# Optimization experiments

Measured on AMD Instinct MI355X. Metric: run time of the kernel, lower is better.

Reference implementation:

```python
import jax, jax.numpy as jnp
import numpy as np


def setup_inputs() -> dict:
    key = jax.random.key(0)
    ks = jax.random.split(key, 6)
    bs, n_src, n_tgt = 4, 4096, 16384
    c_src, c_tgt = 256, 128
    xyz_target = jax.random.uniform(ks[0], (bs, n_tgt, 3), dtype=jnp.float32)
    xyz_source = jax.random.uniform(ks[1], (bs, n_src, 3), dtype=jnp.float32)
    feats_target = jax.random.normal(ks[2], (bs, n_tgt, c_tgt), dtype=jnp.float32)
    feats_source = jax.random.normal(ks[3], (bs, n_src, c_src), dtype=jnp.float32)
    # SharedMlP 1x1 conv weights (1,1,cin,cout) squeezed to (cin,cout)
    w1 = jax.random.normal(ks[4], (c_src + c_tgt, 256), dtype=jnp.float32) * (1.0 / np.sqrt(c_src + c_tgt))
    w2 = jax.random.normal(ks[5], (256, 256), dtype=jnp.float32) * (1.0 / np.sqrt(256))
    return {"xyz_target": xyz_target, "xyz_source": xyz_source,
            "feats_target": feats_target, "feats_source": feats_source,
            "w1": w1, "w2": w2}


def reference(xyz_target, xyz_source, feats_target, feats_source, w1, w2):
    # --- three_nn: full pairwise euclidean distance [bs, n_tgt, n_src] ---
    diff = xyz_target[:, :, None, :] - xyz_source[:, None, :, :]
    dis = jnp.linalg.norm(diff, axis=-1)                      # bs, n_tgt, n_src
    neg_dis, idx = jax.lax.top_k(-dis, 3)                     # 3 nearest
    nn_dis = jnp.maximum(-neg_dis, 1e-10)                     # bs, n_tgt, 3
    inv = 1.0 / nn_dis
    weight = inv / jnp.sum(inv, axis=-1, keepdims=True)       # bs, n_tgt, 3
    # --- three_interpolate: batched gather + weighted reduce ---
    feats_sel = jax.vmap(lambda f, i: f[i])(feats_source, idx)  # bs, n_tgt, 3, c
    w_sum = jnp.sum(weight, axis=-1, keepdims=True) + 1e-6
    interp = jnp.einsum('btk,btkc->btc', weight, feats_sel) / w_sum
    # --- concat skip features, 1x1-conv MLP (pointwise matmul) ---
    x = jnp.concatenate([interp, feats_target], axis=2)       # bs, n_tgt, 384
    x = jax.nn.relu(jnp.einsum('btc,cd->btd', x, w1))
    x = jax.nn.relu(jnp.einsum('btc,cd->btd', x, w2))
    return x
```

## Files before the change

### kernel.cpp

```cpp
#include <hip/hip_runtime.h>
#include <hip/hip_bf16.h>
#include <stdint.h>

#define BS 4
#define NS 4096
#define NT 16384
#define CS 256
#define CT 128
#define KC1 384
#define NOUT 256
#define MTOT (BS*NT)
#define GR 8
#define NC (GR*GR*GR)
#define HCELL 0.125f

typedef __attribute__((ext_vector_type(4))) float floatx4;
typedef __attribute__((ext_vector_type(8))) short shortx8;
typedef __attribute__((ext_vector_type(8))) __bf16 bf16x8;

__device__ __forceinline__ unsigned short f2bf(float f) {
  unsigned int u = __builtin_bit_cast(unsigned int, f);
  u += 0x7FFFu + ((u >> 16) & 1u);
  return (unsigned short)(u >> 16);
}

__device__ __forceinline__ int cell_of(float x) {
  int c = (int)(x * 8.0f);
  return min(7, max(0, c));
}

__global__ __launch_bounds__(256) void wt_kernel(const float* __restrict__ w1,
    const float* __restrict__ w2, unsigned short* __restrict__ w1t,
    unsigned short* __restrict__ w2t) {
  int i = blockIdx.x * 256 + threadIdx.x;
  if (i < KC1 * NOUT) {
    int n = i / KC1, k = i - n * KC1;
    w1t[i] = f2bf(w1[k * NOUT + n]);
  }
  if (i < NOUT * NOUT) {
    int n = i >> 8, k = i & 255;
    w2t[i] = f2bf(w2[k * NOUT + n]);
  }
}

__global__ __launch_bounds__(512) void bucket_src(const float* __restrict__ xyzs,
    float4* __restrict__ bsrc, int* __restrict__ soff) {
  __shared__ int cnt[NC];
  __shared__ int scan[NC];
  int tid = threadIdx.x;
  int b = blockIdx.x;
  const float* src = xyzs + (size_t)b * NS * 3;
  cnt[tid] = 0;
  __syncthreads();
  #pragma unroll
  for (int k = 0; k < 8; ++k) {
    int p = k * 512 + tid;
    float x = src[3*p], y = src[3*p+1], z = src[3*p+2];
    int c = (cell_of(z) * GR + cell_of(y)) * GR + cell_of(x);
    atomicAdd(&cnt[c], 1);
  }
  __syncthreads();
  scan[tid] = cnt[tid];
  __syncthreads();
  for (int off = 1; off < NC; off <<= 1) {
    int v = (tid >= off) ? scan[tid - off] : 0;
    __syncthreads();
    scan[tid] += v;
    __syncthreads();
  }
  int excl = scan[tid] - cnt[tid];
  cnt[tid] = excl;
  soff[b * (NC + 1) + tid] = excl;
  if (tid == 0) soff[b * (NC + 1) + NC] = NS;
  __syncthreads();
  #pragma unroll
  for (int k = 0; k < 8; ++k) {
    int p = k * 512 + tid;
    float x = src[3*p], y = src[3*p+1], z = src[3*p+2];
    int c = (cell_of(z) * GR + cell_of(y)) * GR + cell_of(x);
    int slot = atomicAdd(&cnt[c], 1);
    bsrc[(size_t)b * NS + slot] = make_float4(x, y, z, __int_as_float(p));
  }
}

__global__ __launch_bounds__(1024) void sort_tgt(const float* __restrict__ xyzt,
    float4* __restrict__ stgt) {
  __shared__ int cnt[NC];
  __shared__ int scan[NC];
  int tid = threadIdx.x;
  int b = blockIdx.x;
  const float* tp = xyzt + (size_t)b * NT * 3;
  if (tid < NC) cnt[tid] = 0;
  __syncthreads();
  #pragma unroll
  for (int k = 0; k < 16; ++k) {
    int p = k * 1024 + tid;
    float x = tp[3*p], y = tp[3*p+1], z = tp[3*p+2];
    int c = (cell_of(z) * GR + cell_of(y)) * GR + cell_of(x);
    atomicAdd(&cnt[c], 1);
  }
  __syncthreads();
  if (tid < NC) scan[tid] = cnt[tid];
  __syncthreads();
  for (int off = 1; off < NC; off <<= 1) {
    int v = (tid < NC && tid >= off) ? scan[tid - off] : 0;
    __syncthreads();
    if (tid < NC) scan[tid] += v;
    __syncthreads();
  }
  if (tid < NC) cnt[tid] = scan[tid] - cnt[tid];
  __syncthreads();
  #pragma unroll
  for (int k = 0; k < 16; ++k) {
    int p = k * 1024 + tid;
    float x = tp[3*p], y = tp[3*p+1], z = tp[3*p+2];
    int c = (cell_of(z) * GR + cell_of(y)) * GR + cell_of(x);
    int slot = atomicAdd(&cnt[c], 1);
    stgt[(size_t)b * NT + slot] = make_float4(x, y, z, __int_as_float(p));
  }
}

__device__ __forceinline__ void ins3(float sc, int jj,
    float& d0, float& d1, float& d2, int& i0, int& i1, int& i2) {
  bool l0 = sc < d0, l1 = sc < d1, l2 = sc < d2;
  d2 = l1 ? d1 : (l2 ? sc : d2);
  i2 = l1 ? i1 : (l2 ? jj : i2);
  d1 = l0 ? d0 : (l1 ? sc : d1);
  i1 = l0 ? i0 : (l1 ? jj : i1);
  d0 = l0 ? sc : d0;
  i0 = l0 ? jj : i0;
}

__device__ __forceinline__ void pair_merge(float& d0, float& d1, float& d2,
                                           int& i0, int& i1, int& i2,
                                           int delta, int sub) {
  float e0 = __shfl_xor(d0, delta);
  float e1 = __shfl_xor(d1, delta);
  float e2 = __shfl_xor(d2, delta);
  int   y0 = __shfl_xor(i0, delta);
  int   y1 = __shfl_xor(i1, delta);
  int   y2 = __shfl_xor(i2, delta);
  float a0,a1,a2,b0,b1,b2; int x0,x1,x2,z0,z1,z2;
  if ((sub & delta) == 0) { a0=d0;a1=d1;a2=d2; x0=i0;x1=i1;x2=i2;
                            b0=e0;b1=e1;b2=e2; z0=y0;z1=y1;z2=y2; }
  else                    { a0=e0;a1=e1;a2=e2; x0=y0;x1=y1;x2=y2;
                            b0=d0;b1=d1;b2=d2; z0=i0;z1=i1;z2=i2; }
  bool t = a0 <= b0;
  d0 = t ? a0 : b0; i0 = t ? x0 : z0;
  float na0 = t ? a1 : a0; int nx0 = t ? x1 : x0;
  float na1 = t ? a2 : a1; int nx1 = t ? x2 : x1;
  float nb0 = t ? b0 : b1; int nz0 = t ? z0 : z1;
  float nb1 = t ? b1 : b2; int nz1 = t ? z1 : z2;
  t = na0 <= nb0;
  d1 = t ? na0 : nb0; i1 = t ? nx0 : nz0;
  float ma0 = t ? na1 : na0; int mx0 = t ? nx1 : nx0;
  float mb0 = t ? nb0 : nb1; int mz0 = t ? nz0 : nz1;
  t = ma0 <= mb0;
  d2 = t ? ma0 : mb0; i2 = t ? mx0 : mz0;
}

__global__ __launch_bounds__(256) void nn_kernel(const float4* __restrict__ stgt,
    const float4* __restrict__ bsrc, const int* __restrict__ soff,
    int* __restrict__ idx_out, float* __restrict__ w_out) {
  __shared__ float4 s_src[NS];
  __shared__ int s_off[NC + 1];
  int tid = threadIdx.x;
  int b = blockIdx.x >> 7;
  int tseg = blockIdx.x & 127;
  for (int i = tid; i < NS; i += 256) s_src[i] = bsrc[(size_t)b * NS + i];
  for (int i = tid; i < NC + 1; i += 256) s_off[i] = soff[b * (NC + 1) + i];
  __syncthreads();
  int tpair = tid >> 1, half = tid & 1;
  float4 tg = stgt[(size_t)b * NT + tseg * 128 + tpair];
  float tx = tg.x, ty = tg.y, tz = tg.z;
  int orig = __float_as_int(tg.w);
  int cx = cell_of(tx), cy = cell_of(ty), cz = cell_of(tz);
  int wx = min(max(cx, 1), 6) - 1;
  int wy = min(max(cy, 1), 6) - 1;
  int wz = min(max(cz, 1), 6) - 1;
  float d0 = 1e30f, d1 = 1e30f, d2 = 1e30f;
  int i0 = 0, i1 = 0, i2 = 0;
  for (int r = half; r < 9; r += 2) {
    int ez = wz + r / 3, ey = wy + r % 3;
    int rowc = (ez * GR + ey) * GR + wx;
    int lo = s_off[rowc], hi = s_off[rowc + 3];
    for (int p = lo; p < hi; ++p) {
      float4 s = s_src[p];
      float dx = tx - s.x, dy = ty - s.y, dz = tz - s.z;
      float q = dx*dx + dy*dy + dz*dz;
      ins3(q, __float_as_int(s.w), d0, d1, d2, i0, i1, i2);
    }
  }
  pair_merge(d0, d1, d2, i0, i1, i2, 1, half);
  float clx = fminf(wx > 0 ? tx - wx * HCELL : 1e30f,
                    wx + 3 < GR ? (wx + 3) * HCELL - tx : 1e30f);
  float cly = fminf(wy > 0 ? ty - wy * HCELL : 1e30f,
                    wy + 3 < GR ? (wy + 3) * HCELL - ty : 1e30f);
  float clz = fminf(wz > 0 ? tz - wz * HCELL : 1e30f,
                    wz + 3 < GR ? (wz + 3) * HCELL - tz : 1e30f);
  float cl = fminf(clx, fminf(cly, clz));
  bool bad = d2 > cl * cl;
  if (__any(bad)) {
    if (bad) {
      d0 = d1 = d2 = 1e30f; i0 = i1 = i2 = 0;
      for (int p = half; p < NS; p += 2) {
        float4 s = s_src[p];
        float dx = tx - s.x, dy = ty - s.y, dz = tz - s.z;
        float q = dx*dx + dy*dy + dz*dz;
        ins3(q, __float_as_int(s.w), d0, d1, d2, i0, i1, i2);
      }
    }
    pair_merge(d0, d1, d2, i0, i1, i2, 1, half);
  }
  if (half == 0) {
    float r0 = fmaxf(sqrtf(d0), 1e-10f);
    float r1 = fmaxf(sqrtf(d1), 1e-10f);
    float r2 = fmaxf(sqrtf(d2), 1e-10f);
    float v0 = 1.f/r0, v1 = 1.f/r1, v2 = 1.f/r2;
    float sc = 1.f / ((v0 + v1 + v2) * (1.f + 1e-6f));
    size_t o = ((size_t)b * NT + orig) * 3;
    idx_out[o] = i0; idx_out[o+1] = i1; idx_out[o+2] = i2;
    w_out[o] = v0*sc; w_out[o+1] = v1*sc; w_out[o+2] = v2*sc;
  }
}

__global__ __launch_bounds__(256) void build_x(const float* __restrict__ ft,
    const float* __restrict__ fs, const int* __restrict__ idxb,
    const float* __restrict__ wgtb, unsigned short* __restrict__ X) {
  int row = blockIdx.x * 4 + (threadIdx.x >> 6);
  int lane = threadIdx.x & 63;
  int b = row >> 14;
  int t = row & (NT - 1);
  const int* ip = idxb + (size_t)row * 3;
  const float* wp = wgtb + (size_t)row * 3;
  int i0 = ip[0], i1 = ip[1], i2 = ip[2];
  float w0 = wp[0], w1 = wp[1], w2 = wp[2];
  const float* fsb = fs + (size_t)b * NS * CS;
  float4 a = *((const float4*)(fsb + (size_t)i0 * CS) + lane);
  float4 c = *((const float4*)(fsb + (size_t)i1 * CS) + lane);
  float4 e = *((const float4*)(fsb + (size_t)i2 * CS) + lane);
  float4 v;
  v.x = w0*a.x + w1*c.x + w2*e.x;
  v.y = w0*a.y + w1*c.y + w2*e.y;
  v.z = w0*a.z + w1*c.z + w2*e.z;
  v.w = w0*a.w + w1*c.w + w2*e.w;
  unsigned short* xr = X + (size_t)row * KC1;
  ushort4 pk; pk.x = f2bf(v.x); pk.y = f2bf(v.y); pk.z = f2bf(v.z); pk.w = f2bf(v.w);
  *(ushort4*)(xr + lane*4) = pk;
  float2 tv = *((const float2*)(ft + ((size_t)b*NT + t)*CT) + lane);
  ushort2 pk2; pk2.x = f2bf(tv.x); pk2.y = f2bf(tv.y);
  *(ushort2*)(xr + CS + lane*2) = pk2;
}

template<int K, bool OUT_BF16>
__global__ __launch_bounds__(256) void mlp_gemm(const unsigned short* __restrict__ A,
    const unsigned short* __restrict__ Bt, void* __restrict__ Cout) {
  constexpr int LDT = 72;
  __shared__ __attribute__((aligned(16))) short sA[128 * LDT];
  __shared__ __attribute__((aligned(16))) short sB[128 * LDT];
  int tid = threadIdx.x;
  int m0 = blockIdx.x * 128;
  int n0 = blockIdx.y * 128;
  int wave = tid >> 6, lane = tid & 63;
  int wm = (wave >> 1) * 64, wn = (wave & 1) * 64;
  int fr = lane & 15, quad = lane >> 4;
  floatx4 zero = {0.f, 0.f, 0.f, 0.f};
  floatx4 acc[4][4];
  #pragma unroll
  for (int i = 0; i < 4; ++i)
    #pragma unroll
    for (int j = 0; j < 4; ++j) acc[i][j] = zero;

  for (int kt = 0; kt < K; kt += 64) {
    #pragma unroll
    for (int i = 0; i < 4; ++i) {
      int chunk = tid + 256 * i;
      int r = chunk >> 3, kc = chunk & 7;
      *(shortx8*)&sA[r * LDT + kc * 8] =
          *(const shortx8*)(A + (size_t)(m0 + r) * K + kt + kc * 8);
      *(shortx8*)&sB[r * LDT + kc * 8] =
          *(const shortx8*)(Bt + (size_t)(n0 + r) * K + kt + kc * 8);
    }
    __syncthreads();
    #pragma unroll
    for (int kk = 0; kk < 64; kk += 32) {
      bf16x8 af[4], bfr[4];
      #pragma unroll
      for (int mi = 0; mi < 4; ++mi)
        af[mi] = __builtin_bit_cast(bf16x8,
            *(const shortx8*)&sA[(wm + mi*16 + fr)*LDT + kk + quad*8]);
      #pragma unroll
      for (int ni = 0; ni < 4; ++ni)
        bfr[ni] = __builtin_bit_cast(bf16x8,
            *(const shortx8*)&sB[(wn + ni*16 + fr)*LDT + kk + quad*8]);
      #pragma unroll
      for (int mi = 0; mi < 4; ++mi)
        #pragma unroll
        for (int ni = 0; ni < 4; ++ni)
          acc[mi][ni] = __builtin_amdgcn_mfma_f32_16x16x32_bf16(
              af[mi], bfr[ni], acc[mi][ni], 0, 0, 0);
    }
    __syncthreads();
  }
  #pragma unroll
  for (int mi = 0; mi < 4; ++mi) {
    #pragma unroll
    for (int ni = 0; ni < 4; ++ni) {
      #pragma unroll
      for (int r = 0; r < 4; ++r) {
        int grow = m0 + wm + mi*16 + quad*4 + r;
        int gcol = n0 + wn + ni*16 + fr;
        float v = fmaxf(acc[mi][ni][r], 0.f);
        if constexpr (OUT_BF16)
          ((unsigned short*)Cout)[(size_t)grow * NOUT + gcol] = f2bf(v);
        else
          ((float*)Cout)[(size_t)grow * NOUT + gcol] = v;
      }
    }
  }
}

extern "C" void kernel_launch(void* const* d_in, const int* in_sizes, int n_in,
                              void* d_out, int out_size, void* d_ws, size_t ws_size,
                              hipStream_t stream) {
  (void)in_sizes; (void)n_in; (void)out_size; (void)ws_size;
  const float* xyzt = (const float*)d_in[0];
  const float* xyzs = (const float*)d_in[1];
  const float* ft   = (const float*)d_in[2];
  const float* fs   = (const float*)d_in[3];
  const float* w1   = (const float*)d_in[4];
  const float* w2   = (const float*)d_in[5];

  char* p = (char*)d_ws;
  unsigned short* w1t = (unsigned short*)p; p += (size_t)KC1*NOUT*2;
  unsigned short* w2t = (unsigned short*)p; p += (size_t)NOUT*NOUT*2;
  int*   idxb = (int*)p;   p += (size_t)MTOT*3*4;
  float* wgtb = (float*)p; p += (size_t)MTOT*3*4;
  unsigned short* Xb = (unsigned short*)p; p += (size_t)MTOT*KC1*2;
  unsigned short* Y1 = (unsigned short*)p; p += (size_t)MTOT*NOUT*2;

  char* q = (char*)Xb;
  float4* bsrc = (float4*)q;              q += (size_t)BS*NS*16;
  float4* stgt = (float4*)q;              q += (size_t)BS*NT*16;
  int*    soff = (int*)q;

  hipLaunchKernelGGL(wt_kernel, dim3(384), dim3(256), 0, stream, w1, w2, w1t, w2t);
  hipLaunchKernelGGL(bucket_src, dim3(BS), dim3(512), 0, stream, xyzs, bsrc, soff);
  hipLaunchKernelGGL(sort_tgt, dim3(BS), dim3(1024), 0, stream, xyzt, stgt);
  hipLaunchKernelGGL(nn_kernel, dim3(512), dim3(256), 0, stream, stgt, bsrc, soff, idxb, wgtb);
  hipLaunchKernelGGL(build_x, dim3(MTOT/4), dim3(256), 0, stream, ft, fs, idxb, wgtb, Xb);
  hipLaunchKernelGGL((mlp_gemm<KC1, true>),  dim3(MTOT/128, 2), dim3(256), 0, stream, Xb, w1t, (void*)Y1);
  hipLaunchKernelGGL((mlp_gemm<NOUT, false>), dim3(MTOT/128, 2), dim3(256), 0, stream, Y1, w2t, d_out);
}
```

Before: 228.4 us.

## Precompute source features times W1 before interpolation and fuse the MLP layers

Uses linearity to multiply the source features by the first 256 rows of W1 once per source point (16K rows instead of 64K target rows). The three-neighbour weighted gather is then applied to these projected rows inside a fused kernel. That kernel adds the target-feature GEMM, applies ReLU, and runs the second layer from shared memory, so the X and Y1 intermediates never go to HBM. It adds an extra bf16 rounding of G before interpolation, which slightly changes numerics, and each block reloads the full W1b and W2 tiles.

```diff
diff --git a/kernel.cpp b/kernel.cpp
--- a/kernel.cpp
+++ b/kernel.cpp
@@ -7,7 +7,6 @@
 #define NT 16384
 #define CS 256
 #define CT 128
-#define KC1 384
 #define NOUT 256
 #define MTOT (BS*NT)
 #define GR 8
@@ -16,6 +15,7 @@
 
 typedef __attribute__((ext_vector_type(4))) float floatx4;
 typedef __attribute__((ext_vector_type(8))) short shortx8;
+typedef __attribute__((ext_vector_type(8))) unsigned short ushortx8;
 typedef __attribute__((ext_vector_type(8))) __bf16 bf16x8;
 
 __device__ __forceinline__ unsigned short f2bf(float f) {
@@ -23,23 +23,26 @@
   u += 0x7FFFu + ((u >> 16) & 1u);
   return (unsigned short)(u >> 16);
 }
-
+__device__ __forceinline__ float bf2f(unsigned short u) {
+  return __builtin_bit_cast(float, ((unsigned int)u) << 16);
+}
 __device__ __forceinline__ int cell_of(float x) {
   int c = (int)(x * 8.0f);
   return min(7, max(0, c));
 }
 
 __global__ __launch_bounds__(256) void wt_kernel(const float* __restrict__ w1,
-    const float* __restrict__ w2, unsigned short* __restrict__ w1t,
-    unsigned short* __restrict__ w2t) {
+    const float* __restrict__ w2, unsigned short* __restrict__ w1at,
+    unsigned short* __restrict__ w1bt, unsigned short* __restrict__ w2t) {
   int i = blockIdx.x * 256 + threadIdx.x;
-  if (i < KC1 * NOUT) {
-    int n = i / KC1, k = i - n * KC1;
-    w1t[i] = f2bf(w1[k * NOUT + n]);
-  }
-  if (i < NOUT * NOUT) {
+  {
     int n = i >> 8, k = i & 255;
-    w2t[i] = f2bf(w2[k * NOUT + n]);
+    w1at[i] = f2bf(w1[k * NOUT + n]);
+    w2t[i]  = f2bf(w2[k * NOUT + n]);
+  }
+  if (i < 256 * 128) {
+    int n = i >> 7, k = i & 127;
+    w1bt[i] = f2bf(w1[(256 + k) * NOUT + n]);
   }
 }
 
@@ -224,40 +227,11 @@
   }
 }
 
-__global__ __launch_bounds__(256) void build_x(const float* __restrict__ ft,
-    const float* __restrict__ fs, const int* __restrict__ idxb,
-    const float* __restrict__ wgtb, unsigned short* __restrict__ X) {
-  int row = blockIdx.x * 4 + (threadIdx.x >> 6);
-  int lane = threadIdx.x & 63;
-  int b = row >> 14;
-  int t = row & (NT - 1);
-  const int* ip = idxb + (size_t)row * 3;
-  const float* wp = wgtb + (size_t)row * 3;
-  int i0 = ip[0], i1 = ip[1], i2 = ip[2];
-  float w0 = wp[0], w1 = wp[1], w2 = wp[2];
-  const float* fsb = fs + (size_t)b * NS * CS;
-  float4 a = *((const float4*)(fsb + (size_t)i0 * CS) + lane);
-  float4 c = *((const float4*)(fsb + (size_t)i1 * CS) + lane);
-  float4 e = *((const float4*)(fsb + (size_t)i2 * CS) + lane);
-  float4 v;
-  v.x = w0*a.x + w1*c.x + w2*e.x;
-  v.y = w0*a.y + w1*c.y + w2*e.y;
-  v.z = w0*a.z + w1*c.z + w2*e.z;
-  v.w = w0*a.w + w1*c.w + w2*e.w;
-  unsigned short* xr = X + (size_t)row * KC1;
-  ushort4 pk; pk.x = f2bf(v.x); pk.y = f2bf(v.y); pk.z = f2bf(v.z); pk.w = f2bf(v.w);
-  *(ushort4*)(xr + lane*4) = pk;
-  float2 tv = *((const float2*)(ft + ((size_t)b*NT + t)*CT) + lane);
-  ushort2 pk2; pk2.x = f2bf(tv.x); pk2.y = f2bf(tv.y);
-  *(ushort2*)(xr + CS + lane*2) = pk2;
-}
-
-template<int K, bool OUT_BF16>
-__global__ __launch_bounds__(256) void mlp_gemm(const unsigned short* __restrict__ A,
-    const unsigned short* __restrict__ Bt, void* __restrict__ Cout) {
+__global__ __launch_bounds__(256) void gemm_g(const float* __restrict__ fs,
+    const unsigned short* __restrict__ w1at, unsigned short* __restrict__ G) {
   constexpr int LDT = 72;
-  __shared__ __attribute__((aligned(16))) short sA[128 * LDT];
-  __shared__ __attribute__((aligned(16))) short sB[128 * LDT];
+  __shared__ __attribute__((aligned(16))) unsigned short sA[128 * LDT];
+  __shared__ __attribute__((aligned(16))) unsigned short sB[128 * LDT];
   int tid = threadIdx.x;
   int m0 = blockIdx.x * 128;
   int n0 = blockIdx.y * 128;
@@ -271,15 +245,25 @@
     #pragma unroll
     for (int j = 0; j < 4; ++j) acc[i][j] = zero;
 
-  for (int kt = 0; kt < K; kt += 64) {
+  for (int kt = 0; kt < 256; kt += 64) {
     #pragma unroll
     for (int i = 0; i < 4; ++i) {
-      int chunk = tid + 256 * i;
-      int r = chunk >> 3, kc = chunk & 7;
-      *(shortx8*)&sA[r * LDT + kc * 8] =
-          *(const shortx8*)(A + (size_t)(m0 + r) * K + kt + kc * 8);
-      *(shortx8*)&sB[r * LDT + kc * 8] =
-          *(const shortx8*)(Bt + (size_t)(n0 + r) * K + kt + kc * 8);
+      int u = tid + 256 * i;
+      int r = u >> 3, k8 = (u & 7) * 8;
+      const float* src = fs + (size_t)(m0 + r) * 256 + kt + k8;
+      float4 f0 = *(const float4*)src;
+      float4 f1 = *(const float4*)(src + 4);
+      ushortx8 o;
+      o[0]=f2bf(f0.x); o[1]=f2bf(f0.y); o[2]=f2bf(f0.z); o[3]=f2bf(f0.w);
+      o[4]=f2bf(f1.x); o[5]=f2bf(f1.y); o[6]=f2bf(f1.z); o[7]=f2bf(f1.w);
+      *(ushortx8*)&sA[r * LDT + k8] = o;
+    }
+    #pragma unroll
+    for (int i = 0; i < 4; ++i) {
+      int u = tid + 256 * i;
+      int n = u >> 3, kc = (u & 7) * 8;
+      *(ushortx8*)&sB[n * LDT + kc] =
+          *(const ushortx8*)(w1at + (size_t)(n0 + n) * 256 + kt + kc);
     }
     __syncthreads();
     #pragma unroll
@@ -288,11 +272,11 @@
       #pragma unroll
       for (int mi = 0; mi < 4; ++mi)
         af[mi] = __builtin_bit_cast(bf16x8,
-            *(const shortx8*)&sA[(wm + mi*16 + fr)*LDT + kk + quad*8]);
+            *(const ushortx8*)&sA[(wm + mi*16 + fr)*LDT + kk + quad*8]);
       #pragma unroll
       for (int ni = 0; ni < 4; ++ni)
         bfr[ni] = __builtin_bit_cast(bf16x8,
-            *(const shortx8*)&sB[(wn + ni*16 + fr)*LDT + kk + quad*8]);
+            *(const ushortx8*)&sB[(wn + ni*16 + fr)*LDT + kk + quad*8]);
       #pragma unroll
       for (int mi = 0; mi < 4; ++mi)
         #pragma unroll
@@ -303,21 +287,162 @@
     __syncthreads();
   }
   #pragma unroll
-  for (int mi = 0; mi < 4; ++mi) {
-    #pragma unroll
-    for (int ni = 0; ni < 4; ++ni) {
+  for (int mi = 0; mi < 4; ++mi)
+    #pragma unroll
+    for (int ni = 0; ni < 4; ++ni)
       #pragma unroll
       for (int r = 0; r < 4; ++r) {
         int grow = m0 + wm + mi*16 + quad*4 + r;
         int gcol = n0 + wn + ni*16 + fr;
-        float v = fmaxf(acc[mi][ni][r], 0.f);
-        if constexpr (OUT_BF16)
-          ((unsigned short*)Cout)[(size_t)grow * NOUT + gcol] = f2bf(v);
-        else
-          ((float*)Cout)[(size_t)grow * NOUT + gcol] = v;
+        G[(size_t)grow * 256 + gcol] = f2bf(acc[mi][ni][r]);
       }
-    }
-  }
+}
+
+__global__ __launch_bounds__(256) void fused_mlp(const float* __restrict__ ft,
+    const unsigned short* __restrict__ G, const int* __restrict__ idxb,
+    const float* __restrict__ wgtb, const unsigned short* __restrict__ w1bt,
+    const unsigned short* __restrict__ w2t, float* __restrict__ out) {
+  constexpr int LDI = 264;
+  constexpr int LDT = 72;
+  __shared__ __attribute__((aligned(16))) unsigned short sI[64 * LDI];
+  __shared__ __attribute__((aligned(16))) unsigned short sA[64 * LDT];
+  __shared__ __attribute__((aligned(16))) unsigned short sB[256 * LDT];
+  int tid = threadIdx.x;
+  int row0 = blockIdx.x * 64;
+  int b = row0 >> 14;
+  int wave = tid >> 6, lane = tid & 63;
+  int wn = wave * 64;
+  int fr = lane & 15, quad = lane >> 4;
+
+  {
+    int r = tid >> 2, seg = tid & 3;
+    int grow = row0 + r;
+    const int* ip = idxb + (size_t)grow * 3;
+    const float* wp = wgtb + (size_t)grow * 3;
+    int g0i = ip[0], g1i = ip[1], g2i = ip[2];
+    float w0 = wp[0], w1v = wp[1], w2v = wp[2];
+    const unsigned short* Gb = G + ((size_t)b << 20);
+    const unsigned short* g0 = Gb + ((size_t)g0i << 8) + seg * 64;
+    const unsigned short* g1 = Gb + ((size_t)g1i << 8) + seg * 64;
+    const unsigned short* g2 = Gb + ((size_t)g2i << 8) + seg * 64;
+    #pragma unroll
+    for (int j = 0; j < 8; ++j) {
+      ushortx8 a = *(const ushortx8*)(g0 + j*8);
+      ushortx8 c = *(const ushortx8*)(g1 + j*8);
+      ushortx8 e = *(const ushortx8*)(g2 + j*8);
+      ushortx8 o;
+      #pragma unroll
+      for (int q = 0; q < 8; ++q)
+        o[q] = f2bf(w0*bf2f(a[q]) + w1v*bf2f(c[q]) + w2v*bf2f(e[q]));
+      *(ushortx8*)&sI[r * LDI + seg * 64 + j * 8] = o;
+    }
+  }
+
+  floatx4 zero = {0.f, 0.f, 0.f, 0.f};
+  floatx4 acc[4][4];
+  #pragma unroll
+  for (int i = 0; i < 4; ++i)
+    #pragma unroll
+    for (int j = 0; j < 4; ++j) acc[i][j] = zero;
+
+  for (int kt = 0; kt < 128; kt += 64) {
+    #pragma unroll
+    for (int i = 0; i < 2; ++i) {
+      int u = tid + 256 * i;
+      int r = u >> 3, k8 = (u & 7) * 8;
+      const float* src = ft + (size_t)(row0 + r) * CT + kt + k8;
+      float4 f0 = *(const float4*)src;
+      float4 f1 = *(const float4*)(src + 4);
+      ushortx8 o;
+      o[0]=f2bf(f0.x); o[1]=f2bf(f0.y); o[2]=f2bf(f0.z); o[3]=f2bf(f0.w);
+      o[4]=f2bf(f1.x); o[5]=f2bf(f1.y); o[6]=f2bf(f1.z); o[7]=f2bf(f1.w);
+      *(ushortx8*)&sA[r * LDT + k8] = o;
+    }
+    #pragma unroll
+    for (int i = 0; i < 8; ++i) {
+      int u = tid + 256 * i;
+      int n = u >> 3, kc = (u & 7) * 8;
+      *(ushortx8*)&sB[n * LDT + kc] =
+          *(const ushortx8*)(w1bt + (size_t)n * CT + kt + kc);
+    }
+    __syncthreads();
+    #pragma unroll
+    for (int kk = 0; kk < 64; kk += 32) {
+      bf16x8 af[4], bfr[4];
+      #pragma unroll
+      for (int mi = 0; mi < 4; ++mi)
+        af[mi] = __builtin_bit_cast(bf16x8,
+            *(const ushortx8*)&sA[(mi*16 + fr)*LDT + kk + quad*8]);
+      #pragma unroll
+      for (int ni = 0; ni < 4; ++ni)
+        bfr[ni] = __builtin_bit_cast(bf16x8,
+            *(const ushortx8*)&sB[(wn + ni*16 + fr)*LDT + kk + quad*8]);
+      #pragma unroll
+      for (int mi = 0; mi < 4; ++mi)
+        #pragma unroll
+        for (int ni = 0; ni < 4; ++ni)
+          acc[mi][ni] = __builtin_amdgcn_mfma_f32_16x16x32_bf16(
+              af[mi], bfr[ni], acc[mi][ni], 0, 0, 0);
+    }
+    __syncthreads();
+  }
+
+  #pragma unroll
+  for (int mi = 0; mi < 4; ++mi)
+    #pragma unroll
+    for (int ni = 0; ni < 4; ++ni)
+      #pragma unroll
+      for (int r = 0; r < 4; ++r) {
+        int lr = mi*16 + quad*4 + r;
+        int lc = wn + ni*16 + fr;
+        float v = acc[mi][ni][r] + bf2f(sI[lr * LDI + lc]);
+        sI[lr * LDI + lc] = f2bf(fmaxf(v, 0.f));
+      }
+  __syncthreads();
+
+  #pragma unroll
+  for (int i = 0; i < 4; ++i)
+    #pragma unroll
+    for (int j = 0; j < 4; ++j) acc[i][j] = zero;
+  for (int kt = 0; kt < 256; kt += 64) {
+    #pragma unroll
+    for (int i = 0; i < 8; ++i) {
+      int u = tid + 256 * i;
+      int n = u >> 3, kc = (u & 7) * 8;
+      *(ushortx8*)&sB[n * LDT + kc] =
+          *(const ushortx8*)(w2t + (size_t)n * 256 + kt + kc);
+    }
+    __syncthreads();
+    #pragma unroll
+    for (int kk = 0; kk < 64; kk += 32) {
+      bf16x8 af[4], bfr[4];
+      #pragma unroll
+      for (int mi = 0; mi < 4; ++mi)
+        af[mi] = __builtin_bit_cast(bf16x8,
+            *(const ushortx8*)&sI[(mi*16 + fr)*LDI + kt + kk + quad*8]);
+      #pragma unroll
+      for (int ni = 0; ni < 4; ++ni)
+        bfr[ni] = __builtin_bit_cast(bf16x8,
+            *(const ushortx8*)&sB[(wn + ni*16 + fr)*LDT + kk + quad*8]);
+      #pragma unroll
+      for (int mi = 0; mi < 4; ++mi)
+        #pragma unroll
+        for (int ni = 0; ni < 4; ++ni)
+          acc[mi][ni] = __builtin_amdgcn_mfma_f32_16x16x32_bf16(
+              af[mi], bfr[ni], acc[mi][ni], 0, 0, 0);
+    }
+    __syncthreads();
+  }
+  #pragma unroll
+  for (int mi = 0; mi < 4; ++mi)
+    #pragma unroll
+    for (int ni = 0; ni < 4; ++ni)
+      #pragma unroll
+      for (int r = 0; r < 4; ++r) {
+        int grow = row0 + mi*16 + quad*4 + r;
+        int gcol = wn + ni*16 + fr;
+        out[(size_t)grow * 256 + gcol] = fmaxf(acc[mi][ni][r], 0.f);
+      }
 }
 
 extern "C" void kernel_launch(void* const* d_in, const int* in_sizes, int n_in,
@@ -332,23 +457,21 @@
   const float* w2   = (const float*)d_in[5];
 
   char* p = (char*)d_ws;
-  unsigned short* w1t = (unsigned short*)p; p += (size_t)KC1*NOUT*2;
-  unsigned short* w2t = (unsigned short*)p; p += (size_t)NOUT*NOUT*2;
+  unsigned short* w1at = (unsigned short*)p; p += (size_t)256*256*2;
+  unsigned short* w1bt = (unsigned short*)p; p += (size_t)256*128*2;
+  unsigned short* w2t  = (unsigned short*)p; p += (size_t)256*256*2;
   int*   idxb = (int*)p;   p += (size_t)MTOT*3*4;
   float* wgtb = (float*)p; p += (size_t)MTOT*3*4;
-  unsigned short* Xb = (unsigned short*)p; p += (size_t)MTOT*KC1*2;
-  unsigned short* Y1 = (unsigned short*)p; p += (size_t)MTOT*NOUT*2;
-
-  char* q = (char*)Xb;
-  float4* bsrc = (float4*)q;              q += (size_t)BS*NS*16;
-  float4* stgt = (float4*)q;              q += (size_t)BS*NT*16;
-  int*    soff = (int*)q;
-
-  hipLaunchKernelGGL(wt_kernel, dim3(384), dim3(256), 0, stream, w1, w2, w1t, w2t);
+  unsigned short* G = (unsigned short*)p; p += (size_t)BS*NS*NOUT*2;
+  float4* bsrc = (float4*)p; p += (size_t)BS*NS*16;
+  float4* stgt = (float4*)p; p += (size_t)BS*NT*16;
+  int*    soff = (int*)p;
+
+  hipLaunchKernelGGL(wt_kernel, dim3(256), dim3(256), 0, stream, w1, w2, w1at, w1bt, w2t);
   hipLaunchKernelGGL(bucket_src, dim3(BS), dim3(512), 0, stream, xyzs, bsrc, soff);
   hipLaunchKernelGGL(sort_tgt, dim3(BS), dim3(1024), 0, stream, xyzt, stgt);
   hipLaunchKernelGGL(nn_kernel, dim3(512), dim3(256), 0, stream, stgt, bsrc, soff, idxb, wgtb);
-  hipLaunchKernelGGL(build_x, dim3(MTOT/4), dim3(256), 0, stream, ft, fs, idxb, wgtb, Xb);
-  hipLaunchKernelGGL((mlp_gemm<KC1, true>),  dim3(MTOT/128, 2), dim3(256), 0, stream, Xb, w1t, (void*)Y1);
-  hipLaunchKernelGGL((mlp_gemm<NOUT, false>), dim3(MTOT/128, 2), dim3(256), 0, stream, Y1, w2t, d_out);
-}
+  hipLaunchKernelGGL(gemm_g, dim3(BS*NS/128, 2), dim3(256), 0, stream, fs, w1at, G);
+  hipLaunchKernelGGL(fused_mlp, dim3(MTOT/64), dim3(256), 0, stream,
+                     ft, G, idxb, wgtb, w1bt, w2t, (float*)d_out);
+}
```

New measurement: 211.5 us. 1.08x faster.
